# Kernel tuning notes

Hardware: AMD Instinct MI355X
Metric: run time of the kernel (lower is better)

## Reference

```python
import jax, jax.numpy as jnp
import numpy as np
from jax import lax

DEPTH, DIM, HEADS, DHEAD = 4, 384, 8, 64
INNER = HEADS * DHEAD          # 512
HID = int(DIM * 0.25)          # 96 (hardcoded in Transformer_Conv)
B, Hg, Wg = 8, 32, 32
N = Hg * Wg
SCALE = DHEAD ** -0.5
EPS = 1e-5


def _layer_norm(x, w, b):
    mu = jnp.mean(x, axis=-1, keepdims=True)
    var = jnp.mean(jnp.square(x - mu), axis=-1, keepdims=True)
    return (x - mu) * lax.rsqrt(var + EPS) * w + b


def setup_inputs() -> dict:
    key = jax.random.key(0)
    ks = jax.random.split(key, 8)
    s = 0.02
    return {
        "x": jax.random.normal(ks[0], (B, N, DIM), jnp.float32),
        "ln1_w": jnp.ones((DEPTH, DIM), jnp.float32),
        "ln1_b": jnp.zeros((DEPTH, DIM), jnp.float32),
        "w_qkv": jax.random.normal(ks[1], (DEPTH, DIM, 3 * INNER), jnp.float32) * s,
        "w_out": jax.random.normal(ks[2], (DEPTH, INNER, DIM), jnp.float32) * s,
        "b_out": jnp.zeros((DEPTH, DIM), jnp.float32),
        "ln2_w": jnp.ones((DEPTH, DIM), jnp.float32),
        "ln2_b": jnp.zeros((DEPTH, DIM), jnp.float32),
        "fc1_w": jax.random.normal(ks[3], (DEPTH, DIM, HID), jnp.float32) * s,
        "fc1_b": jnp.zeros((DEPTH, HID), jnp.float32),
        "dw_w": jax.random.normal(ks[4], (DEPTH, HID, 1, 3, 3), jnp.float32) * s,
        "dw_b": jnp.zeros((DEPTH, HID), jnp.float32),
        "fc2_w": jax.random.normal(ks[5], (DEPTH, HID, DIM), jnp.float32) * s,
        "fc2_b": jnp.zeros((DEPTH, DIM), jnp.float32),
        "H": Hg,
        "W": Wg,
    }


def _forward(x, ln1_w, ln1_b, w_qkv, w_out, b_out, ln2_w, ln2_b,
             fc1_w, fc1_b, dw_w, dw_b, fc2_w, fc2_b, H, W):
    b, n, c = x.shape
    attn_last = None
    for l in range(DEPTH):
        # ---- PreNorm + Attention (with post-softmax cross-layer residual) ----
        xn = _layer_norm(x, ln1_w[l], ln1_b[l])
        qkv = xn @ w_qkv[l]                                   # [b, n, 3*inner]
        q, k, v = jnp.split(qkv, 3, axis=-1)
        q = q.reshape(b, n, HEADS, DHEAD).transpose(0, 2, 1, 3)  # bhnd
        k = k.reshape(b, n, HEADS, DHEAD).transpose(0, 2, 1, 3)
        v = v.reshape(b, n, HEADS, DHEAD).transpose(0, 2, 1, 3)
        dots = jnp.einsum("bhid,bhjd->bhij", q, k) * SCALE
        attn = jax.nn.softmax(dots, axis=-1)
        if attn_last is not None:
            attn = attn + attn_last
        attn_last = attn
        out = jnp.einsum("bhij,bhjd->bhid", attn, v)
        out = out.transpose(0, 2, 1, 3).reshape(b, n, INNER)
        x = out @ w_out[l] + b_out[l] + x
        # ---- ConvFFN: LN -> fc1 -> depthwise conv 3x3 -> GELU -> fc2 ----
        y = _layer_norm(x, ln2_w[l], ln2_b[l])
        y = y @ fc1_w[l] + fc1_b[l]                            # [b, n, HID]
        y4 = y.transpose(0, 2, 1).reshape(b, HID, H, W)
        y4 = lax.conv_general_dilated(
            y4, dw_w[l], window_strides=(1, 1), padding="SAME",
            feature_group_count=HID,
            dimension_numbers=("NCHW", "OIHW", "NCHW"),
        ) + dw_b[l][None, :, None, None]
        y = y4.reshape(b, HID, n).transpose(0, 2, 1)
        y = jax.nn.gelu(y, approximate=False)                  # torch nn.GELU (erf)
        x = y @ fc2_w[l] + fc2_b[l] + x
    return x


def reference(x, ln1_w, ln1_b, w_qkv, w_out, b_out, ln2_w, ln2_b,
              fc1_w, fc1_b, dw_w, dw_b, fc2_w, fc2_b, H, W):
    return _forward(x, ln1_w, ln1_b, w_qkv, w_out, b_out, ln2_w, ln2_b,
                    fc1_w, fc1_b, dw_w, dw_b, fc2_w, fc2_b, H, W)
```

## Files before the change

kernel.cpp:

```cpp
#include <hip/hip_runtime.h>
#include <hip/hip_bf16.h>
#include <math.h>

#define DEPTH 4
#define DIM 384
#define HEADS 8
#define DHEAD 64
#define INNER 512
#define HID 96
#define BATCH 8
#define NTOK 1024
#define ROWS (BATCH*NTOK)

typedef __attribute__((ext_vector_type(8))) _Float16 half8;
typedef __attribute__((ext_vector_type(4))) _Float16 half4;
typedef __attribute__((ext_vector_type(4))) float f32x4;


__global__ __launch_bounds__(256) void ln_kernel(const float* __restrict__ x,
                                                 const float* __restrict__ w,
                                                 const float* __restrict__ b,
                                                 _Float16* __restrict__ outF) {
  const int row = blockIdx.x * 4 + (threadIdx.x >> 6);
  const int lane = threadIdx.x & 63;
  const float* xr = x + (size_t)row * DIM;
  float v[6];
  float s = 0.f;
#pragma unroll
  for (int i = 0; i < 6; ++i) {
    v[i] = xr[lane + i * 64];
    s += v[i];
  }
#pragma unroll
  for (int m = 1; m < 64; m <<= 1) s += __shfl_xor(s, m);
  const float mean = s * (1.0f / DIM);
  float sq = 0.f;
#pragma unroll
  for (int i = 0; i < 6; ++i) {
    v[i] -= mean;
    sq += v[i] * v[i];
  }
#pragma unroll
  for (int m = 1; m < 64; m <<= 1) sq += __shfl_xor(sq, m);
  const float rs = rsqrtf(sq * (1.0f / DIM) + 1e-5f);
  const int f = row >> 4, lr = row & 15;
#pragma unroll
  for (int i = 0; i < 6; ++i) {
    const int k = lane + i * 64;
    outF[(((size_t)f * 12 + (k >> 5)) * 16 + lr) * 32 + (k & 31)] =
        (_Float16)(v[i] * rs * w[k] + b[k]);
  }
}

__global__ __launch_bounds__(256) void transposeW(const float* __restrict__ in0,
                                                  _Float16* __restrict__ out0,
                                                  int K, int N, int Npad) {
  __shared__ float t[32][33];
  const int l = blockIdx.z;
  const int KS = K >> 5;
  const float* in = in0 + (size_t)l * K * N;
  _Float16* out = out0 + (size_t)l * Npad * K;
  const int k0 = blockIdx.x * 32, n0 = blockIdx.y * 32;
  const int tx = threadIdx.x & 31, ty = threadIdx.x >> 5;
#pragma unroll
  for (int i = 0; i < 4; ++i) {
    int k = k0 + ty + i * 8, n = n0 + tx;
    t[ty + i * 8][tx] = (n < N) ? in[(size_t)k * N + n] : 0.f;
  }
  __syncthreads();
  const int k = k0 + tx;
#pragma unroll
  for (int i = 0; i < 4; ++i) {
    int n = n0 + ty + i * 8;
    if (n < Npad)
      out[(((size_t)(n >> 4) * KS + (k >> 5)) * 16 + (n & 15)) * 32 + (k & 31)] =
          (_Float16)t[tx][ty + i * 8];
  }
}

template <bool BIAS, bool RES, bool OUT16, int KT, int NT>
__global__ __launch_bounds__(256) void hgemm(const _Float16* __restrict__ AF,
                                             const _Float16* __restrict__ BF,
                                             const float* __restrict__ bias,
                                             const float* __restrict__ res,
                                             void* __restrict__ Cout) {
  constexpr int KS = KT / 32;
  const int tid = threadIdx.x;
  const int wave = tid >> 6, lane = tid & 63;
  const int wm = wave >> 1, wn = wave & 1;
  const int g = lane >> 4, lr = lane & 15;
  const int m0 = blockIdx.x * 128 + wm * 64;
  const int n0 = blockIdx.y * 128 + wn * 64;
  const int fA = m0 >> 4, fB = n0 >> 4;
  const int lo = lr * 32 + g * 8;
  f32x4 acc[4][4];
#pragma unroll
  for (int i = 0; i < 4; ++i)
#pragma unroll
    for (int j = 0; j < 4; ++j) acc[i][j] = {0.f, 0.f, 0.f, 0.f};

  for (int ks = 0; ks < KS; ++ks) {
    half8 af[4], bf[4];
#pragma unroll
    for (int i = 0; i < 4; ++i)
      af[i] = *(const half8*)(AF + ((size_t)(fA + i) * KS + ks) * 512 + lo);
#pragma unroll
    for (int j = 0; j < 4; ++j)
      bf[j] = *(const half8*)(BF + ((size_t)(fB + j) * KS + ks) * 512 + lo);
#pragma unroll
    for (int i = 0; i < 4; ++i)
#pragma unroll
      for (int j = 0; j < 4; ++j)
        acc[i][j] =
            __builtin_amdgcn_mfma_f32_16x16x32_f16(af[i], bf[j], acc[i][j], 0, 0, 0);
  }

#pragma unroll
  for (int i = 0; i < 4; ++i) {
#pragma unroll
    for (int j = 0; j < 4; ++j) {
      const int n = n0 + j * 16 + lr;
      if (NT % 128 == 0 || n < NT) {
        float bb = BIAS ? bias[n] : 0.f;
#pragma unroll
        for (int jj = 0; jj < 4; ++jj) {
          const int m = m0 + i * 16 + g * 4 + jj;
          float v = acc[i][j][jj] + bb;
          const size_t idx = (size_t)m * NT + n;
          if (RES) v += res[idx];
          if (OUT16)
            ((_Float16*)Cout)[idx] = (_Float16)v;
          else
            ((float*)Cout)[idx] = v;
        }
      }
    }
  }
}

__global__ __launch_bounds__(256) void hgemm_fc1(const _Float16* __restrict__ AF,
                                                 const _Float16* __restrict__ BF,
                                                 const float* __restrict__ bias,
                                                 _Float16* __restrict__ C) {
  const int tid = threadIdx.x;
  const int wave = tid >> 6, lane = tid & 63;
  const int g = lane >> 4, lr = lane & 15;
  const int m0 = blockIdx.x * 32;
  const int fA = m0 >> 4, fB = wave * 2;
  const int lo = lr * 32 + g * 8;
  f32x4 acc[2][2];
#pragma unroll
  for (int i = 0; i < 2; ++i)
#pragma unroll
    for (int j = 0; j < 2; ++j) acc[i][j] = {0.f, 0.f, 0.f, 0.f};

  for (int ks = 0; ks < 12; ++ks) {
    half8 af[2], bf[2];
#pragma unroll
    for (int i = 0; i < 2; ++i)
      af[i] = *(const half8*)(AF + ((size_t)(fA + i) * 12 + ks) * 512 + lo);
#pragma unroll
    for (int j = 0; j < 2; ++j)
      bf[j] = *(const half8*)(BF + ((size_t)(fB + j) * 12 + ks) * 512 + lo);
#pragma unroll
    for (int i = 0; i < 2; ++i)
#pragma unroll
      for (int j = 0; j < 2; ++j)
        acc[i][j] =
            __builtin_amdgcn_mfma_f32_16x16x32_f16(af[i], bf[j], acc[i][j], 0, 0, 0);
  }

#pragma unroll
  for (int i = 0; i < 2; ++i)
#pragma unroll
    for (int j = 0; j < 2; ++j) {
      const int n = wave * 32 + j * 16 + lr;
      if (n < HID) {
        const float bb = bias[n];
#pragma unroll
        for (int jj = 0; jj < 4; ++jj) {
          const int m = m0 + i * 16 + g * 4 + jj;
          C[(size_t)m * HID + n] = (_Float16)(acc[i][j][jj] + bb);
        }
      }
    }
}

__global__ __launch_bounds__(256) void hgemm_qkv(const _Float16* __restrict__ AF,
                                                 const _Float16* __restrict__ BF,
                                                 _Float16* __restrict__ qF,
                                                 _Float16* __restrict__ kT,
                                                 _Float16* __restrict__ vTn) {
  const int tid = threadIdx.x;
  const int wave = tid >> 6, lane = tid & 63;
  const int wm = wave >> 1, wn = wave & 1;
  const int g = lane >> 4, lr = lane & 15;
  const int m0 = blockIdx.x * 128 + wm * 64;
  const int n0 = blockIdx.y * 128 + wn * 64;
  const int fA = m0 >> 4, fB = n0 >> 4;
  const int lo = lr * 32 + g * 8;
  f32x4 acc[4][4];
#pragma unroll
  for (int i = 0; i < 4; ++i)
#pragma unroll
    for (int j = 0; j < 4; ++j) acc[i][j] = {0.f, 0.f, 0.f, 0.f};

  for (int ks = 0; ks < 12; ++ks) {
    half8 af[4], bf[4];
#pragma unroll
    for (int i = 0; i < 4; ++i)
      af[i] = *(const half8*)(AF + ((size_t)(fA + i) * 12 + ks) * 512 + lo);
#pragma unroll
    for (int j = 0; j < 4; ++j)
      bf[j] = *(const half8*)(BF + ((size_t)(fB + j) * 12 + ks) * 512 + lo);
#pragma unroll
    for (int i = 0; i < 4; ++i)
#pragma unroll
      for (int j = 0; j < 4; ++j)
        acc[i][j] =
            __builtin_amdgcn_mfma_f32_16x16x32_f16(af[i], bf[j], acc[i][j], 0, 0, 0);
  }

  if (n0 < 512) {
#pragma unroll
    for (int i = 0; i < 4; ++i)
#pragma unroll
      for (int j = 0; j < 4; ++j) {
        const int n = n0 + j * 16 + lr;
#pragma unroll
        for (int jj = 0; jj < 4; ++jj) {
          const int m = m0 + i * 16 + g * 4 + jj;
          qF[(((size_t)(m >> 4) * 16 + (n >> 5)) * 16 + (m & 15)) * 32 + (n & 31)] =
              (_Float16)acc[i][j][jj];
        }
      }
  } else if (n0 < 1024) {
#pragma unroll
    for (int j = 0; j < 4; ++j) {
      const int n = n0 + j * 16 + lr;
      const int hk = (n - 512) >> 6, d = (n - 512) & 63;
      const int sb = d >> 5, dd = d & 31;
#pragma unroll
      for (int i = 0; i < 4; ++i)
#pragma unroll
        for (int jj = 0; jj < 4; ++jj) {
          const int m = m0 + i * 16 + g * 4 + jj;
          const int bb = m >> 10, tok = m & 1023;
          const int f = tok >> 4, tr = tok & 15;
          kT[((((size_t)(bb * 8 + hk) * 64 + f) * 2 + sb) * 16 + tr) * 32 + dd] =
              (_Float16)acc[i][j][jj];
        }
    }
  } else {
    const int bb = m0 >> 10;
    const int tok0 = (m0 & 1023) + g * 4;
#pragma unroll
    for (int j = 0; j < 4; ++j) {
      const int dg = n0 + j * 16 + lr - 1024;
      const int hk = dg >> 6, d = dg & 63;
#pragma unroll
      for (int i = 0; i < 4; ++i) {
        const int tok = tok0 + i * 16;
        const int kb = tok >> 5, tk = tok & 31;
        half4 t = {(_Float16)acc[i][j][0], (_Float16)acc[i][j][1],
                   (_Float16)acc[i][j][2], (_Float16)acc[i][j][3]};
        *(half4*)(vTn + (((size_t)(bb * 8 + hk) * 32 + kb) * 64 + d) * 32 + tk) = t;
      }
    }
  }
}

__device__ __forceinline__ int pidx(int r, int c) {
  return ((((r << 11) + (c << 1)) ^ ((r & 15) << 4)) >> 1);
}

__global__ __launch_bounds__(512) void attn_kernel(
    const _Float16* __restrict__ qF, const _Float16* __restrict__ kT,
    const _Float16* __restrict__ vTn, _Float16* __restrict__ store,
    _Float16* __restrict__ aoutF, int has_prev, int write_store) {
  __shared__ __align__(16) char smem[32768];
  _Float16* P = (_Float16*)smem;
  float (*red)[16][68] = (float (*)[16][68])smem;
  __shared__ __align__(16) float partial[8][16];

  const int tid = threadIdx.x;
  const int wave = tid >> 6, lane = tid & 63;
  const int g = lane >> 4, lr = lane & 15;
  const int blk = blockIdx.x;
  const int xcd = blk & 7, j0 = blk >> 3;
  const int bh = xcd * 8 + (j0 >> 6), rt = j0 & 63;
  const int b = bh >> 3, h = bh & 7;
  const int r0 = rt << 4;
  const int fq = (b * NTOK + r0) >> 4;

  const _Float16* kbase = kT + (size_t)bh * 64 * 1024;
  const _Float16* vbase = vTn + (size_t)bh * 32 * 2048;
  const size_t gbase = ((size_t)bh * 64 + rt) * 16384;
  const int fragoff = lr * 16 + g * 4;

  half4 prev4[8];
  if (has_prev) {
#pragma unroll
    for (int fl = 0; fl < 8; ++fl)
      prev4[fl] = *(const half4*)(store + gbase +
                                  (size_t)(wave * 8 + fl) * 256 + fragoff);
  }

  const half8 a0 =
      *(const half8*)(qF + (((size_t)fq * 16 + h * 2) * 16 + lr) * 32 + g * 8);
  const half8 a1 = *(const half8*)(
      qF + (((size_t)fq * 16 + h * 2 + 1) * 16 + lr) * 32 + g * 8);

  float p[8][4];
  float rs[4] = {0.f, 0.f, 0.f, 0.f};
  __builtin_amdgcn_s_setprio(1);
#pragma unroll
  for (int fl = 0; fl < 8; ++fl) {
    const int f = wave * 8 + fl;
    const _Float16* kb = kbase + (size_t)f * 1024 + lr * 32 + g * 8;
    half8 b0 = *(const half8*)(kb);
    half8 b1 = *(const half8*)(kb + 512);
    f32x4 acc = {0.f, 0.f, 0.f, 0.f};
    acc = __builtin_amdgcn_mfma_f32_16x16x32_f16(a0, b0, acc, 0, 0, 0);
    acc = __builtin_amdgcn_mfma_f32_16x16x32_f16(a1, b1, acc, 0, 0, 0);
#pragma unroll
    for (int j = 0; j < 4; ++j) {
      float e = __expf(acc[j] * 0.125f);
      p[fl][j] = e;
      rs[j] += e;
    }
  }
  __builtin_amdgcn_s_setprio(0);
#pragma unroll
  for (int j = 0; j < 4; ++j) {
    rs[j] += __shfl_xor(rs[j], 1);
    rs[j] += __shfl_xor(rs[j], 2);
    rs[j] += __shfl_xor(rs[j], 4);
    rs[j] += __shfl_xor(rs[j], 8);
  }
  if (lr == 0) {
#pragma unroll
    for (int j = 0; j < 4; ++j) partial[wave][g * 4 + j] = rs[j];
  }
  __syncthreads();

  f32x4 sv = {0.f, 0.f, 0.f, 0.f};
#pragma unroll
  for (int w = 0; w < 8; ++w) {
    const float4 pw = *(const float4*)&partial[w][g * 4];
    sv[0] += pw.x; sv[1] += pw.y; sv[2] += pw.z; sv[3] += pw.w;
  }
  float inv[4];
#pragma unroll
  for (int j = 0; j < 4; ++j) inv[j] = 1.0f / sv[j];

  half4 t4[8];
#pragma unroll
  for (int fl = 0; fl < 8; ++fl) {
    const int c = wave * 128 + fl * 16 + lr;
#pragma unroll
    for (int j = 0; j < 4; ++j) {
      float val = p[fl][j] * inv[j];
      if (has_prev) val += (float)prev4[fl][j];
      const _Float16 hv = (_Float16)val;
      t4[fl][j] = hv;
      P[pidx(g * 4 + j, c)] = hv;
    }
  }
  __syncthreads();

  const int nf = wave & 3, kh = wave >> 2;
  f32x4 oacc = {0.f, 0.f, 0.f, 0.f};
  __builtin_amdgcn_s_setprio(1);
#pragma unroll
  for (int ks = 0; ks < 16; ++ks) {
    const int kb = kh * 16 + ks;
    half8 af = *(half8*)(P + pidx(lr, kb * 32 + g * 8));
    half8 bfv = *(const half8*)(vbase + ((size_t)kb * 64 + nf * 16 + lr) * 32 + g * 8);
    oacc = __builtin_amdgcn_mfma_f32_16x16x32_f16(af, bfv, oacc, 0, 0, 0);
  }
  __builtin_amdgcn_s_setprio(0);
  __syncthreads();

  if (write_store) {
#pragma unroll
    for (int fl = 0; fl < 8; ++fl)
      *(half4*)(store + gbase + (size_t)(wave * 8 + fl) * 256 + fragoff) =
          t4[fl];
  }

#pragma unroll
  for (int j = 0; j < 4; ++j) red[kh][g * 4 + j][nf * 16 + lr] = oacc[j];
  __syncthreads();
#pragma unroll
  for (int it = 0; it < 2; ++it) {
    const int e = tid + it * 512;
    const int r = e >> 6, d = e & 63;
    float s = red[0][r][d] + red[1][r][d];
    aoutF[(((size_t)fq * 16 + h * 2 + (d >> 5)) * 16 + r) * 32 + (d & 31)] =
        (_Float16)s;
  }
}

__global__ __launch_bounds__(256) void dwconv_gelu(const _Float16* __restrict__ y,
                                                   const float* __restrict__ w,
                                                   const float* __restrict__ bs,
                                                   _Float16* __restrict__ outF) {
  const int blk = blockIdx.x;
  const int bb = blk / 96;
  const int rem = blk - bb * 96;
  const int hh = rem / 3, cg = rem - (rem / 3) * 3;
#pragma unroll
  for (int it = 0; it < 4; ++it) {
    const int e = threadIdx.x + it * 256;
    const int c = cg * 32 + (e & 31), ww = e >> 5;
    float acc = bs[c];
#pragma unroll
    for (int dh = 0; dh < 3; ++dh) {
      int ih = hh + dh - 1;
      if (ih < 0 || ih >= 32) continue;
#pragma unroll
      for (int dw = 0; dw < 3; ++dw) {
        int iw = ww + dw - 1;
        if (iw < 0 || iw >= 32) continue;
        acc += (float)y[((size_t)(bb * NTOK + ih * 32 + iw)) * HID + c] *
               w[c * 9 + dh * 3 + dw];
      }
    }
    float gl = 0.5f * acc * (1.f + erff(acc * 0.70710678118f));
    const int f = bb * 64 + hh * 2 + (ww >> 4);
    outF[(((size_t)f * 3 + cg) * 16 + (ww & 15)) * 32 + (e & 31)] = (_Float16)gl;
  }
}

extern "C" void kernel_launch(void* const* d_in, const int* in_sizes, int n_in,
                              void* d_out, int out_size, void* d_ws,
                              size_t ws_size, hipStream_t stream) {
  const float* x_in  = (const float*)d_in[0];
  const float* ln1_w = (const float*)d_in[1];
  const float* ln1_b = (const float*)d_in[2];
  const float* w_qkv = (const float*)d_in[3];
  const float* w_out = (const float*)d_in[4];
  const float* b_out = (const float*)d_in[5];
  const float* ln2_w = (const float*)d_in[6];
  const float* ln2_b = (const float*)d_in[7];
  const float* fc1_w = (const float*)d_in[8];
  const float* fc1_b = (const float*)d_in[9];
  const float* dw_w  = (const float*)d_in[10];
  const float* dw_b  = (const float*)d_in[11];
  const float* fc2_w = (const float*)d_in[12];
  const float* fc2_b = (const float*)d_in[13];

  float* x = (float*)d_out;

  char* ws = (char*)d_ws;
  _Float16* xnF   = (_Float16*)ws; ws += (size_t)ROWS * DIM * 2;
  _Float16* qF    = (_Float16*)ws; ws += (size_t)ROWS * 512 * 2;
  _Float16* kT    = (_Float16*)ws; ws += (size_t)64 * 64 * 1024 * 2;
  _Float16* vTn   = (_Float16*)ws; ws += (size_t)64 * 32 * 2048 * 2;
  _Float16* aoutF = (_Float16*)ws; ws += (size_t)ROWS * INNER * 2;
  _Float16* y1    = (_Float16*)ws; ws += (size_t)ROWS * HID * 2;
  _Float16* y2F   = (_Float16*)ws; ws += (size_t)ROWS * HID * 2;
  _Float16* wqkvT = (_Float16*)ws; ws += (size_t)DEPTH * 1536 * DIM * 2;
  _Float16* woutT = (_Float16*)ws; ws += (size_t)DEPTH * DIM * INNER * 2;
  _Float16* fc1T  = (_Float16*)ws; ws += (size_t)DEPTH * 128 * DIM * 2;
  _Float16* fc2T  = (_Float16*)ws; ws += (size_t)DEPTH * DIM * HID * 2;
  _Float16* astore = (_Float16*)ws;

  transposeW<<<dim3(12, 48, DEPTH), 256, 0, stream>>>(w_qkv, wqkvT, DIM,
                                                      1536, 1536);
  transposeW<<<dim3(16, 12, DEPTH), 256, 0, stream>>>(w_out, woutT, INNER,
                                                      DIM, DIM);
  transposeW<<<dim3(12, 4, DEPTH), 256, 0, stream>>>(fc1_w, fc1T, DIM, HID,
                                                     128);
  transposeW<<<dim3(3, 12, DEPTH), 256, 0, stream>>>(fc2_w, fc2T, HID, DIM,
                                                     DIM);

  hipMemcpyAsync(x, x_in, (size_t)ROWS * DIM * 4, hipMemcpyDeviceToDevice,
                 stream);

  for (int l = 0; l < DEPTH; ++l) {
    ln_kernel<<<ROWS / 4, 256, 0, stream>>>(x, ln1_w + l * DIM,
                                            ln1_b + l * DIM, xnF);
    hgemm_qkv<<<dim3(64, 12), 256, 0, stream>>>(
        xnF, wqkvT + (size_t)l * 1536 * DIM, qF, kT, vTn);
    attn_kernel<<<4096, 512, 0, stream>>>(qF, kT, vTn, astore, aoutF,
                                          l > 0 ? 1 : 0,
                                          l < DEPTH - 1 ? 1 : 0);
    hgemm<true, true, false, INNER, DIM><<<dim3(64, 3), 256, 0, stream>>>(
        aoutF, woutT + (size_t)l * DIM * INNER, b_out + l * DIM, x, x);
    ln_kernel<<<ROWS / 4, 256, 0, stream>>>(x, ln2_w + l * DIM,
                                            ln2_b + l * DIM, xnF);
    hgemm_fc1<<<ROWS / 32, 256, 0, stream>>>(
        xnF, fc1T + (size_t)l * 128 * DIM, fc1_b + l * HID, y1);
    dwconv_gelu<<<768, 256, 0, stream>>>(y1, dw_w + l * HID * 9,
                                         dw_b + l * HID, y2F);
    hgemm<true, true, false, HID, DIM><<<dim3(64, 3), 256, 0, stream>>>(
        y2F, fc2T + (size_t)l * DIM * HID, fc2_b + l * DIM, x, x);
  }
}
```

Baseline: 652.9 us.

## Keep residual stream in fp16 and process two row tiles per attention block

```diff
diff --git a/kernel.cpp b/kernel.cpp
--- a/kernel.cpp
+++ b/kernel.cpp
@@ -14,22 +14,35 @@
 
 typedef __attribute__((ext_vector_type(8))) _Float16 half8;
 typedef __attribute__((ext_vector_type(4))) _Float16 half4;
+typedef __attribute__((ext_vector_type(2))) _Float16 half2v;
 typedef __attribute__((ext_vector_type(4))) float f32x4;
 
 
-__global__ __launch_bounds__(256) void ln_kernel(const float* __restrict__ x,
+__global__ __launch_bounds__(256) void cvt_kernel(const float* __restrict__ in,
+                                                  _Float16* __restrict__ out) {
+  const int i = blockIdx.x * 256 + threadIdx.x;
+  if (i < ROWS * DIM / 4) {
+    const float4 v = ((const float4*)in)[i];
+    half4 o = {(_Float16)v.x, (_Float16)v.y, (_Float16)v.z, (_Float16)v.w};
+    *(half4*)(out + (size_t)i * 4) = o;
+  }
+}
+
+__global__ __launch_bounds__(256) void ln_kernel(const _Float16* __restrict__ x,
                                                  const float* __restrict__ w,
                                                  const float* __restrict__ b,
                                                  _Float16* __restrict__ outF) {
   const int row = blockIdx.x * 4 + (threadIdx.x >> 6);
   const int lane = threadIdx.x & 63;
-  const float* xr = x + (size_t)row * DIM;
+  const _Float16* xr = x + (size_t)row * DIM;
   float v[6];
   float s = 0.f;
 #pragma unroll
-  for (int i = 0; i < 6; ++i) {
-    v[i] = xr[lane + i * 64];
-    s += v[i];
+  for (int i = 0; i < 3; ++i) {
+    half2v h = *(const half2v*)(xr + i * 128 + lane * 2);
+    v[2 * i] = (float)h[0];
+    v[2 * i + 1] = (float)h[1];
+    s += v[2 * i] + v[2 * i + 1];
   }
 #pragma unroll
   for (int m = 1; m < 64; m <<= 1) s += __shfl_xor(s, m);
@@ -45,10 +58,13 @@
   const float rs = rsqrtf(sq * (1.0f / DIM) + 1e-5f);
   const int f = row >> 4, lr = row & 15;
 #pragma unroll
-  for (int i = 0; i < 6; ++i) {
-    const int k = lane + i * 64;
-    outF[(((size_t)f * 12 + (k >> 5)) * 16 + lr) * 32 + (k & 31)] =
-        (_Float16)(v[i] * rs * w[k] + b[k]);
+  for (int i = 0; i < 3; ++i) {
+#pragma unroll
+    for (int j = 0; j < 2; ++j) {
+      const int k = i * 128 + lane * 2 + j;
+      outF[(((size_t)f * 12 + (k >> 5)) * 16 + lr) * 32 + (k & 31)] =
+          (_Float16)(v[2 * i + j] * rs * w[k] + b[k]);
+    }
   }
 }
 
@@ -82,7 +98,7 @@
 __global__ __launch_bounds__(256) void hgemm(const _Float16* __restrict__ AF,
                                              const _Float16* __restrict__ BF,
                                              const float* __restrict__ bias,
-                                             const float* __restrict__ res,
+                                             const _Float16* __restrict__ res,
                                              void* __restrict__ Cout) {
   constexpr int KS = KT / 32;
   const int tid = threadIdx.x;
@@ -127,7 +143,7 @@
           const int m = m0 + i * 16 + g * 4 + jj;
           float v = acc[i][j][jj] + bb;
           const size_t idx = (size_t)m * NT + n;
-          if (RES) v += res[idx];
+          if (RES) v += (float)res[idx];
           if (OUT16)
             ((_Float16*)Cout)[idx] = (_Float16)v;
           else
@@ -288,117 +304,123 @@
   const int g = lane >> 4, lr = lane & 15;
   const int blk = blockIdx.x;
   const int xcd = blk & 7, j0 = blk >> 3;
-  const int bh = xcd * 8 + (j0 >> 6), rt = j0 & 63;
+  const int bh = xcd * 8 + (j0 >> 5);
+  const int pair = j0 & 31;
   const int b = bh >> 3, h = bh & 7;
-  const int r0 = rt << 4;
-  const int fq = (b * NTOK + r0) >> 4;
 
   const _Float16* kbase = kT + (size_t)bh * 64 * 1024;
   const _Float16* vbase = vTn + (size_t)bh * 32 * 2048;
-  const size_t gbase = ((size_t)bh * 64 + rt) * 16384;
   const int fragoff = lr * 16 + g * 4;
-
-  half4 prev4[8];
-  if (has_prev) {
-#pragma unroll
-    for (int fl = 0; fl < 8; ++fl)
-      prev4[fl] = *(const half4*)(store + gbase +
-                                  (size_t)(wave * 8 + fl) * 256 + fragoff);
-  }
-
-  const half8 a0 =
-      *(const half8*)(qF + (((size_t)fq * 16 + h * 2) * 16 + lr) * 32 + g * 8);
-  const half8 a1 = *(const half8*)(
-      qF + (((size_t)fq * 16 + h * 2 + 1) * 16 + lr) * 32 + g * 8);
-
-  float p[8][4];
-  float rs[4] = {0.f, 0.f, 0.f, 0.f};
-  __builtin_amdgcn_s_setprio(1);
-#pragma unroll
-  for (int fl = 0; fl < 8; ++fl) {
-    const int f = wave * 8 + fl;
-    const _Float16* kb = kbase + (size_t)f * 1024 + lr * 32 + g * 8;
-    half8 b0 = *(const half8*)(kb);
-    half8 b1 = *(const half8*)(kb + 512);
-    f32x4 acc = {0.f, 0.f, 0.f, 0.f};
-    acc = __builtin_amdgcn_mfma_f32_16x16x32_f16(a0, b0, acc, 0, 0, 0);
-    acc = __builtin_amdgcn_mfma_f32_16x16x32_f16(a1, b1, acc, 0, 0, 0);
+  const int nf = wave & 3, kh = wave >> 2;
+
+  for (int t = 0; t < 2; ++t) {
+    const int rt = pair * 2 + t;
+    const int r0 = rt << 4;
+    const int fq = (b * NTOK + r0) >> 4;
+    const size_t gbase = ((size_t)bh * 64 + rt) * 16384;
+
+    half4 prev4[8];
+    if (has_prev) {
+#pragma unroll
+      for (int fl = 0; fl < 8; ++fl)
+        prev4[fl] = *(const half4*)(store + gbase +
+                                    (size_t)(wave * 8 + fl) * 256 + fragoff);
+    }
+
+    const half8 a0 = *(const half8*)(
+        qF + (((size_t)fq * 16 + h * 2) * 16 + lr) * 32 + g * 8);
+    const half8 a1 = *(const half8*)(
+        qF + (((size_t)fq * 16 + h * 2 + 1) * 16 + lr) * 32 + g * 8);
+
+    float p[8][4];
+    float rs[4] = {0.f, 0.f, 0.f, 0.f};
+    __builtin_amdgcn_s_setprio(1);
+#pragma unroll
+    for (int fl = 0; fl < 8; ++fl) {
+      const int f = wave * 8 + fl;
+      const _Float16* kb = kbase + (size_t)f * 1024 + lr * 32 + g * 8;
+      half8 b0 = *(const half8*)(kb);
+      half8 b1 = *(const half8*)(kb + 512);
+      f32x4 acc = {0.f, 0.f, 0.f, 0.f};
+      acc = __builtin_amdgcn_mfma_f32_16x16x32_f16(a0, b0, acc, 0, 0, 0);
+      acc = __builtin_amdgcn_mfma_f32_16x16x32_f16(a1, b1, acc, 0, 0, 0);
+#pragma unroll
+      for (int j = 0; j < 4; ++j) {
+        float e = __expf(acc[j] * 0.125f);
+        p[fl][j] = e;
+        rs[j] += e;
+      }
+    }
+    __builtin_amdgcn_s_setprio(0);
 #pragma unroll
     for (int j = 0; j < 4; ++j) {
-      float e = __expf(acc[j] * 0.125f);
-      p[fl][j] = e;
-      rs[j] += e;
-    }
-  }
-  __builtin_amdgcn_s_setprio(0);
-#pragma unroll
-  for (int j = 0; j < 4; ++j) {
-    rs[j] += __shfl_xor(rs[j], 1);
-    rs[j] += __shfl_xor(rs[j], 2);
-    rs[j] += __shfl_xor(rs[j], 4);
-    rs[j] += __shfl_xor(rs[j], 8);
-  }
-  if (lr == 0) {
-#pragma unroll
-    for (int j = 0; j < 4; ++j) partial[wave][g * 4 + j] = rs[j];
-  }
-  __syncthreads();
-
-  f32x4 sv = {0.f, 0.f, 0.f, 0.f};
-#pragma unroll
-  for (int w = 0; w < 8; ++w) {
-    const float4 pw = *(const float4*)&partial[w][g * 4];
-    sv[0] += pw.x; sv[1] += pw.y; sv[2] += pw.z; sv[3] += pw.w;
-  }
-  float inv[4];
-#pragma unroll
-  for (int j = 0; j < 4; ++j) inv[j] = 1.0f / sv[j];
-
-  half4 t4[8];
-#pragma unroll
-  for (int fl = 0; fl < 8; ++fl) {
-    const int c = wave * 128 + fl * 16 + lr;
-#pragma unroll
-    for (int j = 0; j < 4; ++j) {
-      float val = p[fl][j] * inv[j];
-      if (has_prev) val += (float)prev4[fl][j];
-      const _Float16 hv = (_Float16)val;
-      t4[fl][j] = hv;
-      P[pidx(g * 4 + j, c)] = hv;
-    }
-  }
-  __syncthreads();
-
-  const int nf = wave & 3, kh = wave >> 2;
-  f32x4 oacc = {0.f, 0.f, 0.f, 0.f};
-  __builtin_amdgcn_s_setprio(1);
-#pragma unroll
-  for (int ks = 0; ks < 16; ++ks) {
-    const int kb = kh * 16 + ks;
-    half8 af = *(half8*)(P + pidx(lr, kb * 32 + g * 8));
-    half8 bfv = *(const half8*)(vbase + ((size_t)kb * 64 + nf * 16 + lr) * 32 + g * 8);
-    oacc = __builtin_amdgcn_mfma_f32_16x16x32_f16(af, bfv, oacc, 0, 0, 0);
-  }
-  __builtin_amdgcn_s_setprio(0);
-  __syncthreads();
-
-  if (write_store) {
-#pragma unroll
-    for (int fl = 0; fl < 8; ++fl)
-      *(half4*)(store + gbase + (size_t)(wave * 8 + fl) * 256 + fragoff) =
-          t4[fl];
-  }
-
-#pragma unroll
-  for (int j = 0; j < 4; ++j) red[kh][g * 4 + j][nf * 16 + lr] = oacc[j];
-  __syncthreads();
-#pragma unroll
-  for (int it = 0; it < 2; ++it) {
-    const int e = tid + it * 512;
-    const int r = e >> 6, d = e & 63;
-    float s = red[0][r][d] + red[1][r][d];
-    aoutF[(((size_t)fq * 16 + h * 2 + (d >> 5)) * 16 + r) * 32 + (d & 31)] =
-        (_Float16)s;
+      rs[j] += __shfl_xor(rs[j], 1);
+      rs[j] += __shfl_xor(rs[j], 2);
+      rs[j] += __shfl_xor(rs[j], 4);
+      rs[j] += __shfl_xor(rs[j], 8);
+    }
+    if (lr == 0) {
+#pragma unroll
+      for (int j = 0; j < 4; ++j) partial[wave][g * 4 + j] = rs[j];
+    }
+    __syncthreads();
+
+    f32x4 sv = {0.f, 0.f, 0.f, 0.f};
+#pragma unroll
+    for (int w = 0; w < 8; ++w) {
+      const float4 pw = *(const float4*)&partial[w][g * 4];
+      sv[0] += pw.x; sv[1] += pw.y; sv[2] += pw.z; sv[3] += pw.w;
+    }
+    float inv[4];
+#pragma unroll
+    for (int j = 0; j < 4; ++j) inv[j] = 1.0f / sv[j];
+
+    half4 t4[8];
+#pragma unroll
+    for (int fl = 0; fl < 8; ++fl) {
+      const int c = wave * 128 + fl * 16 + lr;
+#pragma unroll
+      for (int j = 0; j < 4; ++j) {
+        float val = p[fl][j] * inv[j];
+        if (has_prev) val += (float)prev4[fl][j];
+        const _Float16 hv = (_Float16)val;
+        t4[fl][j] = hv;
+        P[pidx(g * 4 + j, c)] = hv;
+      }
+    }
+    __syncthreads();
+
+    f32x4 oacc = {0.f, 0.f, 0.f, 0.f};
+    __builtin_amdgcn_s_setprio(1);
+#pragma unroll
+    for (int ks = 0; ks < 16; ++ks) {
+      const int kb = kh * 16 + ks;
+      half8 af = *(half8*)(P + pidx(lr, kb * 32 + g * 8));
+      half8 bfv =
+          *(const half8*)(vbase + ((size_t)kb * 64 + nf * 16 + lr) * 32 + g * 8);
+      oacc = __builtin_amdgcn_mfma_f32_16x16x32_f16(af, bfv, oacc, 0, 0, 0);
+    }
+    __builtin_amdgcn_s_setprio(0);
+    __syncthreads();
+
+    if (write_store) {
+#pragma unroll
+      for (int fl = 0; fl < 8; ++fl)
+        *(half4*)(store + gbase + (size_t)(wave * 8 + fl) * 256 + fragoff) =
+            t4[fl];
+    }
+
+#pragma unroll
+    for (int j = 0; j < 4; ++j) red[kh][g * 4 + j][nf * 16 + lr] = oacc[j];
+    __syncthreads();
+#pragma unroll
+    for (int it = 0; it < 2; ++it) {
+      const int e = tid + it * 512;
+      const int r = e >> 6, d = e & 63;
+      float s = red[0][r][d] + red[1][r][d];
+      aoutF[(((size_t)fq * 16 + h * 2 + (d >> 5)) * 16 + r) * 32 + (d & 31)] =
+          (_Float16)s;
+    }
   }
 }
 
@@ -451,9 +473,10 @@
   const float* fc2_w = (const float*)d_in[12];
   const float* fc2_b = (const float*)d_in[13];
 
-  float* x = (float*)d_out;
+  float* xout = (float*)d_out;
 
   char* ws = (char*)d_ws;
+  _Float16* x16   = (_Float16*)ws; ws += (size_t)ROWS * DIM * 2;
   _Float16* xnF   = (_Float16*)ws; ws += (size_t)ROWS * DIM * 2;
   _Float16* qF    = (_Float16*)ws; ws += (size_t)ROWS * 512 * 2;
   _Float16* kT    = (_Float16*)ws; ws += (size_t)64 * 64 * 1024 * 2;
@@ -476,26 +499,30 @@
   transposeW<<<dim3(3, 12, DEPTH), 256, 0, stream>>>(fc2_w, fc2T, HID, DIM,
                                                      DIM);
 
-  hipMemcpyAsync(x, x_in, (size_t)ROWS * DIM * 4, hipMemcpyDeviceToDevice,
-                 stream);
+  cvt_kernel<<<(ROWS * DIM / 4 + 255) / 256, 256, 0, stream>>>(x_in, x16);
 
   for (int l = 0; l < DEPTH; ++l) {
-    ln_kernel<<<ROWS / 4, 256, 0, stream>>>(x, ln1_w + l * DIM,
+    ln_kernel<<<ROWS / 4, 256, 0, stream>>>(x16, ln1_w + l * DIM,
                                             ln1_b + l * DIM, xnF);
     hgemm_qkv<<<dim3(64, 12), 256, 0, stream>>>(
         xnF, wqkvT + (size_t)l * 1536 * DIM, qF, kT, vTn);
-    attn_kernel<<<4096, 512, 0, stream>>>(qF, kT, vTn, astore, aoutF,
+    attn_kernel<<<2048, 512, 0, stream>>>(qF, kT, vTn, astore, aoutF,
                                           l > 0 ? 1 : 0,
                                           l < DEPTH - 1 ? 1 : 0);
-    hgemm<true, true, false, INNER, DIM><<<dim3(64, 3), 256, 0, stream>>>(
-        aoutF, woutT + (size_t)l * DIM * INNER, b_out + l * DIM, x, x);
-    ln_kernel<<<ROWS / 4, 256, 0, stream>>>(x, ln2_w + l * DIM,
+    hgemm<true, true, true, INNER, DIM><<<dim3(64, 3), 256, 0, stream>>>(
+        aoutF, woutT + (size_t)l * DIM * INNER, b_out + l * DIM, x16, x16);
+    ln_kernel<<<ROWS / 4, 256, 0, stream>>>(x16, ln2_w + l * DIM,
                                             ln2_b + l * DIM, xnF);
     hgemm_fc1<<<ROWS / 32, 256, 0, stream>>>(
         xnF, fc1T + (size_t)l * 128 * DIM, fc1_b + l * HID, y1);
     dwconv_gelu<<<768, 256, 0, stream>>>(y1, dw_w + l * HID * 9,
                                          dw_b + l * HID, y2F);
-    hgemm<true, true, false, HID, DIM><<<dim3(64, 3), 256, 0, stream>>>(
-        y2F, fc2T + (size_t)l * DIM * HID, fc2_b + l * DIM, x, x);
-  }
-}
+    if (l < DEPTH - 1) {
+      hgemm<true, true, true, HID, DIM><<<dim3(64, 3), 256, 0, stream>>>(
+          y2F, fc2T + (size_t)l * DIM * HID, fc2_b + l * DIM, x16, x16);
+    } else {
+      hgemm<true, true, false, HID, DIM><<<dim3(64, 3), 256, 0, stream>>>(
+          y2F, fc2T + (size_t)l * DIM * HID, fc2_b + l * DIM, x16, xout);
+    }
+  }
+}
```

Result: slower. 862.6 us (+32.1%).
